# Kernel tuning notes

Measured on AMD Instinct MI355X. Metric: run time of the kernel, lower is better.

## Reference

```python
import jax, jax.numpy as jnp
import numpy as np

N = 100000      # nodes
E = 3200000     # edges
IN_DIM = 128
HID = 128
OUT_DIM = 1
LAYERS = 8
ALPHA = 0.1
THETA = 0.5


def setup_inputs() -> dict:
    key = jax.random.key(0)
    ks = jax.random.split(key, 8)
    x = jax.random.normal(ks[0], (N, IN_DIM), dtype=jnp.float32)
    edge_index = jax.random.randint(ks[1], (2, E), 0, N, dtype=jnp.int64)
    edge_weight = jax.random.uniform(ks[2], (E,), dtype=jnp.float32)  # unused by original forward path
    W_in = jax.random.normal(ks[3], (IN_DIM, HID), dtype=jnp.float32) * 0.05
    b_in = jnp.zeros((HID,), dtype=jnp.float32)
    W_gcn = jax.random.normal(ks[4], (LAYERS, HID, HID), dtype=jnp.float32) * 0.05
    W_out = jax.random.normal(ks[5], (HID, OUT_DIM), dtype=jnp.float32) * 0.05
    b_out = jnp.zeros((OUT_DIM,), dtype=jnp.float32)
    return {"x": x, "edge_weight": edge_weight, "W_in": W_in, "b_in": b_in,
            "W_gcn": W_gcn, "W_out": W_out, "b_out": b_out, "edge_index": edge_index}


def _gcn_norm(edge_index, dtype):
    # add self loops (fill value 1), symmetric normalization deg^-1/2 A deg^-1/2
    sl = jnp.arange(N, dtype=edge_index.dtype)
    row = jnp.concatenate([edge_index[0], sl])
    col = jnp.concatenate([edge_index[1], sl])
    w = jnp.ones(row.shape[0], dtype=dtype)
    deg = jax.ops.segment_sum(w, col, num_segments=N)
    dinv = jnp.where(deg > 0, jax.lax.rsqrt(deg), 0.0)
    norm = dinv[row] * dinv[col]
    return row, col, norm


def reference(x, edge_weight, W_in, b_in, W_gcn, W_out, b_out, edge_index):
    row, col, norm = _gcn_norm(edge_index, x.dtype)
    h = x @ W_in + b_in            # initial_proj
    h0 = h                          # residual x0
    for i in range(LAYERS):
        # dropout is identity in eval mode
        msg = h[row] * norm[:, None]                       # gather + scale [E+N, HID]
        agg = jax.ops.segment_sum(msg, col, num_segments=N)
        s = (1.0 - ALPHA) * agg + ALPHA * h0               # identity-mapped residual
        beta = float(np.log(THETA / (i + 1) + 1.0))
        h = (1.0 - beta) * s + beta * (s @ W_gcn[i])       # GCNII weight mix
        h = jax.nn.relu(h)
    return h @ W_out + b_out
```

## Files before the change

kernel.cpp:

```cpp
#include <hip/hip_runtime.h>
#include <hip/hip_bf16.h>
#include <math.h>

#define N_NODES 100000
#define N_EDGES 3200000
#define HID 128
#define LAYERS 8
#define ALPHA 0.1f
#define THETA 0.5f

#define SCAN_TILE 1024
#define NB_SCAN ((N_NODES + SCAN_TILE - 1) / SCAN_TILE)

typedef unsigned int uint;
typedef unsigned short ushort;
typedef __attribute__((ext_vector_type(8))) short short8;
typedef __attribute__((ext_vector_type(4))) float f32x4;

__device__ inline float bf_lo(uint p) { return __uint_as_float(p << 16); }
__device__ inline float bf_hi(uint p) { return __uint_as_float(p & 0xffff0000u); }
__device__ inline uint bf_pack(float x, float y) {
    uint ux = __float_as_uint(x), uy = __float_as_uint(y);
    uint rx = (ux + 0x7fffu + ((ux >> 16) & 1u)) >> 16;
    uint ry = (uy + 0x7fffu + ((uy >> 16) & 1u)) >> 16;
    return rx | (ry << 16);
}
__device__ inline ushort bfr(float x) {
    uint u = __float_as_uint(x);
    return (ushort)((u + 0x7fffu + ((u >> 16) & 1u)) >> 16);
}
__device__ inline float bff(ushort s) { return __uint_as_float(((uint)s) << 16); }

__global__ __launch_bounds__(256) void k_count(const int* __restrict__ col,
                                               int* __restrict__ cnt) {
    int e = blockIdx.x * 256 + threadIdx.x;
    if (e < N_EDGES) atomicAdd(&cnt[col[e]], 1);
}

__global__ __launch_bounds__(256) void k_dinv(const int* __restrict__ cnt,
                                              float* __restrict__ dinv) {
    int n = blockIdx.x * 256 + threadIdx.x;
    if (n < N_NODES) dinv[n] = rsqrtf((float)(cnt[n] + 1));
}

__global__ __launch_bounds__(256) void k_scan1(const int* __restrict__ cnt,
                                               int* __restrict__ indptr,
                                               int* __restrict__ bsum) {
    __shared__ int lds[256];
    int t = threadIdx.x;
    int base = blockIdx.x * SCAN_TILE + t * 4;
    int v[4];
    int s = 0;
#pragma unroll
    for (int j = 0; j < 4; ++j) {
        v[j] = (base + j < N_NODES) ? cnt[base + j] : 0;
        s += v[j];
    }
    lds[t] = s;
    __syncthreads();
    for (int off = 1; off < 256; off <<= 1) {
        int u = (t >= off) ? lds[t - off] : 0;
        __syncthreads();
        lds[t] += u;
        __syncthreads();
    }
    int run = lds[t] - s;
#pragma unroll
    for (int j = 0; j < 4; ++j) {
        if (base + j < N_NODES) indptr[base + j] = run;
        run += v[j];
    }
    if (t == 255) bsum[blockIdx.x] = lds[255];
}

__global__ __launch_bounds__(256) void k_scan2(const int* __restrict__ bsum,
                                               int* __restrict__ boff) {
    __shared__ int lds[256];
    int t = threadIdx.x;
    int v = (t < NB_SCAN) ? bsum[t] : 0;
    lds[t] = v;
    __syncthreads();
    for (int off = 1; off < 256; off <<= 1) {
        int u = (t >= off) ? lds[t - off] : 0;
        __syncthreads();
        lds[t] += u;
        __syncthreads();
    }
    boff[t] = lds[t] - v;
}

__global__ __launch_bounds__(256) void k_scan3(int* __restrict__ indptr,
                                               const int* __restrict__ boff) {
    int base = blockIdx.x * SCAN_TILE + threadIdx.x * 4;
    int add = boff[blockIdx.x];
#pragma unroll
    for (int j = 0; j < 4; ++j) {
        if (base + j < N_NODES) indptr[base + j] += add;
    }
    if (blockIdx.x == 0 && threadIdx.x == 0) indptr[N_NODES] = N_EDGES;
}

__global__ __launch_bounds__(256) void k_fill(const int* __restrict__ rowi,
                                              const int* __restrict__ coli,
                                              const float* __restrict__ dinv,
                                              const int* __restrict__ indptr,
                                              int* __restrict__ cursor,
                                              int2* __restrict__ csr) {
    int e = blockIdx.x * 256 + threadIdx.x;
    if (e >= N_EDGES) return;
    int r = rowi[e];
    int c = coli[e];
    int p = indptr[c] + atomicAdd(&cursor[c], 1);
    csr[p] = make_int2(r, __float_as_int(dinv[r] * dinv[c]));
}

__global__ __launch_bounds__(256) void k_wprep(const float* __restrict__ Wg,
                                               ushort* __restrict__ Wt) {
    int l = blockIdx.x;
    const float* W = Wg + (size_t)l * HID * HID;
    ushort* T = Wt + (size_t)l * HID * HID;
    int t = threadIdx.x;
#pragma unroll
    for (int i = 0; i < 16; ++i) {
        int idx = t + 256 * i;
        int k = idx >> 5;
        int c4 = idx & 31;
        float4 v = *(const float4*)(W + (size_t)k * HID + c4 * 4);
        T[(c4 * 4 + 0) * HID + k] = bfr(v.x);
        T[(c4 * 4 + 1) * HID + k] = bfr(v.y);
        T[(c4 * 4 + 2) * HID + k] = bfr(v.z);
        T[(c4 * 4 + 3) * HID + k] = bfr(v.w);
    }
}

__global__ __launch_bounds__(256) void k_spmm(const uint* __restrict__ h,
                                              const uint* __restrict__ h0,
                                              const float* __restrict__ dinv,
                                              const int* __restrict__ indptr,
                                              const int2* __restrict__ csr,
                                              uint* __restrict__ s_out) {
    int node = blockIdx.x * 4 + (threadIdx.x >> 6);
    if (node >= N_NODES) return;
    int lane = threadIdx.x & 63;
    int beg = indptr[node];
    int end = indptr[node + 1];
    float di = dinv[node];
    uint hs = h[node * 64 + lane];
    uint h0v = h0[node * 64 + lane];
    float ax[8], ay[8];
#pragma unroll
    for (int j = 0; j < 8; ++j) { ax[j] = 0.f; ay[j] = 0.f; }
    int e = beg;
    for (; e + 16 <= end; e += 16) {
        int2 rr[16];
#pragma unroll
        for (int j = 0; j < 16; ++j) rr[j] = csr[e + j];
        uint p[16];
#pragma unroll
        for (int j = 0; j < 16; ++j) p[j] = h[rr[j].x * 64 + lane];
#pragma unroll
        for (int j = 0; j < 16; ++j) {
            float w = __int_as_float(rr[j].y);
            ax[j & 7] = fmaf(w, bf_lo(p[j]), ax[j & 7]);
            ay[j & 7] = fmaf(w, bf_hi(p[j]), ay[j & 7]);
        }
    }
    for (; e < end; e += 4) {
        int2 rr[4];
        float w[4];
#pragma unroll
        for (int j = 0; j < 4; ++j) {
            int idx = e + j;
            rr[j] = csr[idx < end ? idx : beg];
            w[j] = (idx < end) ? __int_as_float(rr[j].y) : 0.f;
        }
        uint p[4];
#pragma unroll
        for (int j = 0; j < 4; ++j) p[j] = h[rr[j].x * 64 + lane];
#pragma unroll
        for (int j = 0; j < 4; ++j) {
            ax[j] = fmaf(w[j], bf_lo(p[j]), ax[j]);
            ay[j] = fmaf(w[j], bf_hi(p[j]), ay[j]);
        }
    }
    float sum0 = ((ax[0] + ax[1]) + (ax[2] + ax[3])) + ((ax[4] + ax[5]) + (ax[6] + ax[7]));
    float sum1 = ((ay[0] + ay[1]) + (ay[2] + ay[3])) + ((ay[4] + ay[5]) + (ay[6] + ay[7]));
    float selfw = di * di;
    float rx = (1.0f - ALPHA) * fmaf(selfw, bf_lo(hs), sum0) + ALPHA * bf_lo(h0v);
    float ry = (1.0f - ALPHA) * fmaf(selfw, bf_hi(hs), sum1) + ALPHA * bf_hi(h0v);
    s_out[node * 64 + lane] = bf_pack(rx, ry);
}

__global__ __launch_bounds__(256) void k_gemm_in(const float* __restrict__ A,
                                                 const float* __restrict__ W,
                                                 const float* __restrict__ bias,
                                                 uint* __restrict__ out0,
                                                 uint* __restrict__ out1) {
    __shared__ float sT[32 * 64];
    __shared__ float Ws[32 * 128];
    int t = threadIdx.x;
    int tr = t & 15;
    int tc = t >> 4;
    int rowBase = blockIdx.x * 64;
    float acc[4][8] = {};

    for (int ko = 0; ko < HID; ko += 32) {
#pragma unroll
        for (int pass = 0; pass < 2; ++pass) {
            int lin = t + 256 * pass;
            int r = lin >> 3;
            int kq = lin & 7;
            int ar = rowBase + r;
            if (ar >= N_NODES) ar = N_NODES - 1;
            float4 v = *(const float4*)(A + (size_t)ar * HID + ko + 4 * kq);
            sT[(4 * kq + 0) * 64 + r] = v.x;
            sT[(4 * kq + 1) * 64 + r] = v.y;
            sT[(4 * kq + 2) * 64 + r] = v.z;
            sT[(4 * kq + 3) * 64 + r] = v.w;
        }
#pragma unroll
        for (int pass = 0; pass < 4; ++pass) {
            int lin = t + 256 * pass;
            int k = lin >> 5;
            int c4 = lin & 31;
            *(float4*)&Ws[k * 128 + 4 * c4] =
                *(const float4*)(W + (size_t)(ko + k) * HID + 4 * c4);
        }
        __syncthreads();
#pragma unroll
        for (int k = 0; k < 32; ++k) {
            float4 a = *(const float4*)&sT[k * 64 + 4 * tr];
            float4 w0 = *(const float4*)&Ws[k * 128 + 8 * tc];
            float4 w1 = *(const float4*)&Ws[k * 128 + 8 * tc + 4];
            float av[4] = {a.x, a.y, a.z, a.w};
            float wv[8] = {w0.x, w0.y, w0.z, w0.w, w1.x, w1.y, w1.z, w1.w};
#pragma unroll
            for (int i = 0; i < 4; ++i)
#pragma unroll
                for (int j = 0; j < 8; ++j)
                    acc[i][j] = fmaf(av[i], wv[j], acc[i][j]);
        }
        __syncthreads();
    }

    int c0 = 8 * tc;
    float bb[8];
#pragma unroll
    for (int j = 0; j < 8; ++j) bb[j] = bias[c0 + j];
#pragma unroll
    for (int i = 0; i < 4; ++i) {
        int r = rowBase + 4 * tr + i;
        if (r >= N_NODES) break;
        float v[8];
#pragma unroll
        for (int j = 0; j < 8; ++j) v[j] = acc[i][j] + bb[j];
        uint4 o;
        o.x = bf_pack(v[0], v[1]);
        o.y = bf_pack(v[2], v[3]);
        o.z = bf_pack(v[4], v[5]);
        o.w = bf_pack(v[6], v[7]);
        *(uint4*)(out0 + (size_t)r * 64 + c0 / 2) = o;
        *(uint4*)(out1 + (size_t)r * 64 + c0 / 2) = o;
    }
}

#define SAS 136

__global__ __launch_bounds__(256) void k_gemm_layer(const uint* __restrict__ A,
                                                    const ushort* __restrict__ Wt,
                                                    uint* __restrict__ out0,
                                                    float beta) {
    __shared__ ushort sA[64 * SAS];
    __shared__ ushort sW[128 * SAS];
    int t = threadIdx.x;
    int lane = t & 63;
    int wv = t >> 6;
    int rowBase = blockIdx.x * 64;

#pragma unroll
    for (int i = 0; i < 4; ++i) {
        int idx = t + 256 * i;
        int r = idx >> 4;
        int q = idx & 15;
        int ar = rowBase + r;
        if (ar >= N_NODES) ar = N_NODES - 1;
        uint4 v = *(const uint4*)(A + (size_t)ar * 64 + q * 4);
        *(uint4*)((uint*)(sA + r * SAS) + q * 4) = v;
    }
#pragma unroll
    for (int i = 0; i < 8; ++i) {
        int idx = t + 256 * i;
        int r = idx >> 4;
        int q = idx & 15;
        uint4 v = *(const uint4*)((const uint*)(Wt + (size_t)r * HID) + q * 4);
        *(uint4*)((uint*)(sW + r * SAS) + q * 4) = v;
    }
    __syncthreads();

    int fr = lane & 15;
    int fq = lane >> 4;
    f32x4 acc[4][2] = {};
#pragma unroll
    for (int kc = 0; kc < 4; ++kc) {
        int kof = kc * 32 + fq * 8;
        short8 b0 = *(const short8*)(sW + (wv * 32 + fr) * SAS + kof);
        short8 b1 = *(const short8*)(sW + (wv * 32 + 16 + fr) * SAS + kof);
#pragma unroll
        for (int tm = 0; tm < 4; ++tm) {
            short8 a = *(const short8*)(sA + (tm * 16 + fr) * SAS + kof);
            acc[tm][0] = __builtin_amdgcn_mfma_f32_16x16x32_bf16(a, b0, acc[tm][0], 0, 0, 0);
            acc[tm][1] = __builtin_amdgcn_mfma_f32_16x16x32_bf16(a, b1, acc[tm][1], 0, 0, 0);
        }
    }
    __syncthreads();

    ushort* pack = sW;
    float ob = 1.0f - beta;
#pragma unroll
    for (int tm = 0; tm < 4; ++tm)
#pragma unroll
        for (int tn = 0; tn < 2; ++tn)
#pragma unroll
            for (int r = 0; r < 4; ++r) {
                int row = tm * 16 + fq * 4 + r;
                int col = wv * 32 + tn * 16 + fr;
                float sv = bff(sA[row * SAS + col]);
                float val = fmaxf(fmaf(ob, sv, beta * acc[tm][tn][r]), 0.f);
                pack[row * 128 + col] = bfr(val);
            }
    __syncthreads();
#pragma unroll
    for (int i = 0; i < 4; ++i) {
        int idx = t + 256 * i;
        int r = idx >> 4;
        int q = idx & 15;
        int ar = rowBase + r;
        if (ar < N_NODES)
            *(uint4*)(out0 + (size_t)ar * 64 + q * 4) =
                *(const uint4*)((const uint*)(pack + r * 128) + q * 4);
    }
}

__global__ __launch_bounds__(256) void k_out(const uint* __restrict__ h,
                                             const float* __restrict__ W_out,
                                             const float* __restrict__ b_out,
                                             float* __restrict__ out) {
    int node = blockIdx.x * 4 + (threadIdx.x >> 6);
    if (node >= N_NODES) return;
    int lane = threadIdx.x & 63;
    uint p = h[node * 64 + lane];
    float2 wv = *(const float2*)(W_out + lane * 2);
    float pr = bf_lo(p) * wv.x + bf_hi(p) * wv.y;
#pragma unroll
    for (int off = 32; off > 0; off >>= 1) pr += __shfl_down(pr, off);
    if (lane == 0) out[node] = pr + b_out[0];
}

extern "C" void kernel_launch(void* const* d_in, const int* in_sizes, int n_in,
                              void* d_out, int out_size, void* d_ws, size_t ws_size,
                              hipStream_t stream) {
    const float* x     = (const float*)d_in[0];
    const float* W_in  = (const float*)d_in[2];
    const float* b_in  = (const float*)d_in[3];
    const float* W_gcn = (const float*)d_in[4];
    const float* W_out = (const float*)d_in[5];
    const float* b_out = (const float*)d_in[6];
    const int*   ei    = (const int*)d_in[7];
    const int* rowi = ei;
    const int* coli = ei + N_EDGES;
    float* out = (float*)d_out;

    char* ws = (char*)d_ws;
    auto alloc = [&](size_t bytes) -> char* {
        char* p = ws;
        ws += (bytes + 255) & ~(size_t)255;
        return p;
    };
    int*    cnt     = (int*)   alloc((size_t)N_NODES * 4);
    float*  dinv    = (float*) alloc((size_t)N_NODES * 4);
    int*    indptr  = (int*)   alloc((size_t)(N_NODES + 1) * 4);
    int*    cursor  = (int*)   alloc((size_t)N_NODES * 4);
    int*    bsum    = (int*)   alloc(1024 * 4);
    int*    boff    = (int*)   alloc(1024 * 4);
    int2*   csr     = (int2*)  alloc((size_t)N_EDGES * 8);
    ushort* Wt      = (ushort*)alloc((size_t)LAYERS * HID * HID * 2);
    uint*   hA      = (uint*)  alloc((size_t)N_NODES * 64 * 4);
    uint*   hB      = (uint*)  alloc((size_t)N_NODES * 64 * 4);
    uint*   h0      = (uint*)  alloc((size_t)N_NODES * 64 * 4);

    hipMemsetAsync(cnt, 0, (size_t)N_NODES * 4, stream);
    hipMemsetAsync(cursor, 0, (size_t)N_NODES * 4, stream);

    k_count<<<(N_EDGES + 255) / 256, 256, 0, stream>>>(coli, cnt);
    k_dinv<<<(N_NODES + 255) / 256, 256, 0, stream>>>(cnt, dinv);
    k_scan1<<<NB_SCAN, 256, 0, stream>>>(cnt, indptr, bsum);
    k_scan2<<<1, 256, 0, stream>>>(bsum, boff);
    k_scan3<<<NB_SCAN, 256, 0, stream>>>(indptr, boff);
    k_fill<<<(N_EDGES + 255) / 256, 256, 0, stream>>>(rowi, coli, dinv, indptr,
                                                      cursor, csr);
    k_wprep<<<LAYERS, 256, 0, stream>>>(W_gcn, Wt);

    int gemm_blocks = (N_NODES + 63) / 64;
    k_gemm_in<<<gemm_blocks, 256, 0, stream>>>(x, W_in, b_in, h0, hA);

    for (int l = 0; l < LAYERS; ++l) {
        k_spmm<<<(N_NODES + 3) / 4, 256, 0, stream>>>(hA, h0, dinv, indptr,
                                                      csr, hB);
        float beta = logf(THETA / (float)(l + 1) + 1.0f);
        k_gemm_layer<<<gemm_blocks, 256, 0, stream>>>(
            hB, Wt + (size_t)l * HID * HID, hA, beta);
    }
    k_out<<<(N_NODES + 3) / 4, 256, 0, stream>>>(hA, W_out, b_out, out);
}
```

Measured before the change: 1.517 ms.

## Fuse SpMM aggregation with per-layer GEMM and pack CSR entries into 32 bits

Each layer now runs one kernel. Every block aggregates 64 nodes' neighbour sums straight into LDS and then does the MFMA weight mix on that tile, so the intermediate s tensor no longer makes a round trip through global memory. CSR entries shrink from int2 to a single uint: a 17-bit source index plus the bf16 normalisation weight with its sign bit dropped, which halves edge-list traffic per layer. In exchange, the 52KB of LDS per block and each wave serially gathering for 16 nodes may lower occupancy and the latency hiding the gather phase depends on. The edge weights are also stored at reduced bf16 precision.

Measured after the change: 1.849 ms. +21.9%, slower.

```diff
diff --git a/kernel.cpp b/kernel.cpp
--- a/kernel.cpp
+++ b/kernel.cpp
@@ -30,6 +30,8 @@
     return (ushort)((u + 0x7fffu + ((u >> 16) & 1u)) >> 16);
 }
 __device__ inline float bff(ushort s) { return __uint_as_float(((uint)s) << 16); }
+
+__device__ inline float rec_w(uint k) { return __uint_as_float((k >> 17) << 16); }
 
 __global__ __launch_bounds__(256) void k_count(const int* __restrict__ col,
                                                int* __restrict__ cnt) {
@@ -105,13 +107,14 @@
                                               const float* __restrict__ dinv,
                                               const int* __restrict__ indptr,
                                               int* __restrict__ cursor,
-                                              int2* __restrict__ csr) {
+                                              uint* __restrict__ csr4) {
     int e = blockIdx.x * 256 + threadIdx.x;
     if (e >= N_EDGES) return;
     int r = rowi[e];
     int c = coli[e];
     int p = indptr[c] + atomicAdd(&cursor[c], 1);
-    csr[p] = make_int2(r, __float_as_int(dinv[r] * dinv[c]));
+    float nrm = dinv[r] * dinv[c];
+    csr4[p] = (uint)r | ((uint)bfr(nrm) << 17);
 }
 
 __global__ __launch_bounds__(256) void k_wprep(const float* __restrict__ Wg,
@@ -133,62 +136,128 @@
     }
 }
 
-__global__ __launch_bounds__(256) void k_spmm(const uint* __restrict__ h,
-                                              const uint* __restrict__ h0,
-                                              const float* __restrict__ dinv,
-                                              const int* __restrict__ indptr,
-                                              const int2* __restrict__ csr,
-                                              uint* __restrict__ s_out) {
-    int node = blockIdx.x * 4 + (threadIdx.x >> 6);
-    if (node >= N_NODES) return;
-    int lane = threadIdx.x & 63;
-    int beg = indptr[node];
-    int end = indptr[node + 1];
-    float di = dinv[node];
-    uint hs = h[node * 64 + lane];
-    uint h0v = h0[node * 64 + lane];
-    float ax[8], ay[8];
-#pragma unroll
-    for (int j = 0; j < 8; ++j) { ax[j] = 0.f; ay[j] = 0.f; }
-    int e = beg;
-    for (; e + 16 <= end; e += 16) {
-        int2 rr[16];
-#pragma unroll
-        for (int j = 0; j < 16; ++j) rr[j] = csr[e + j];
-        uint p[16];
-#pragma unroll
-        for (int j = 0; j < 16; ++j) p[j] = h[rr[j].x * 64 + lane];
-#pragma unroll
-        for (int j = 0; j < 16; ++j) {
-            float w = __int_as_float(rr[j].y);
-            ax[j & 7] = fmaf(w, bf_lo(p[j]), ax[j & 7]);
-            ay[j & 7] = fmaf(w, bf_hi(p[j]), ay[j & 7]);
-        }
-    }
-    for (; e < end; e += 4) {
-        int2 rr[4];
-        float w[4];
-#pragma unroll
-        for (int j = 0; j < 4; ++j) {
-            int idx = e + j;
-            rr[j] = csr[idx < end ? idx : beg];
-            w[j] = (idx < end) ? __int_as_float(rr[j].y) : 0.f;
-        }
-        uint p[4];
-#pragma unroll
-        for (int j = 0; j < 4; ++j) p[j] = h[rr[j].x * 64 + lane];
-#pragma unroll
-        for (int j = 0; j < 4; ++j) {
-            ax[j] = fmaf(w[j], bf_lo(p[j]), ax[j]);
-            ay[j] = fmaf(w[j], bf_hi(p[j]), ay[j]);
-        }
-    }
-    float sum0 = ((ax[0] + ax[1]) + (ax[2] + ax[3])) + ((ax[4] + ax[5]) + (ax[6] + ax[7]));
-    float sum1 = ((ay[0] + ay[1]) + (ay[2] + ay[3])) + ((ay[4] + ay[5]) + (ay[6] + ay[7]));
-    float selfw = di * di;
-    float rx = (1.0f - ALPHA) * fmaf(selfw, bf_lo(hs), sum0) + ALPHA * bf_lo(h0v);
-    float ry = (1.0f - ALPHA) * fmaf(selfw, bf_hi(hs), sum1) + ALPHA * bf_hi(h0v);
-    s_out[node * 64 + lane] = bf_pack(rx, ry);
+#define SAS 136
+
+__global__ __launch_bounds__(256) void k_layer(const uint* __restrict__ h,
+                                               const uint* __restrict__ h0,
+                                               const float* __restrict__ dinv,
+                                               const int* __restrict__ indptr,
+                                               const uint* __restrict__ csr4,
+                                               const ushort* __restrict__ Wt,
+                                               uint* __restrict__ hOut,
+                                               float beta) {
+    __shared__ ushort sA[64 * SAS];
+    __shared__ ushort sW[128 * SAS];
+    int t = threadIdx.x;
+    int lane = t & 63;
+    int wv = t >> 6;
+    int nb = blockIdx.x * 64;
+
+#pragma unroll
+    for (int i = 0; i < 8; ++i) {
+        int idx = t + 256 * i;
+        int r = idx >> 4;
+        int q = idx & 15;
+        uint4 v = *(const uint4*)((const uint*)(Wt + (size_t)r * HID) + q * 4);
+        *(uint4*)((uint*)(sW + r * SAS) + q * 4) = v;
+    }
+
+    for (int i = 0; i < 16; ++i) {
+        int row = wv * 16 + i;
+        int node = nb + row;
+        int nc = node < N_NODES ? node : N_NODES - 1;
+        int beg = indptr[nc];
+        int end = indptr[nc + 1];
+        float di = dinv[nc];
+        uint hs = h[nc * 64 + lane];
+        uint h0v = h0[nc * 64 + lane];
+        float ax[8], ay[8];
+#pragma unroll
+        for (int j = 0; j < 8; ++j) { ax[j] = 0.f; ay[j] = 0.f; }
+        int e = beg;
+        for (; e + 16 <= end; e += 16) {
+            uint kk[16];
+#pragma unroll
+            for (int j = 0; j < 16; ++j) kk[j] = csr4[e + j];
+            uint p[16];
+#pragma unroll
+            for (int j = 0; j < 16; ++j) p[j] = h[(kk[j] & 0x1FFFF) * 64 + lane];
+#pragma unroll
+            for (int j = 0; j < 16; ++j) {
+                float w = rec_w(kk[j]);
+                ax[j & 7] = fmaf(w, bf_lo(p[j]), ax[j & 7]);
+                ay[j & 7] = fmaf(w, bf_hi(p[j]), ay[j & 7]);
+            }
+        }
+        for (; e < end; e += 4) {
+            uint kk[4];
+            float w[4];
+#pragma unroll
+            for (int j = 0; j < 4; ++j) {
+                int idx = e + j;
+                kk[j] = csr4[idx < end ? idx : beg];
+                w[j] = (idx < end) ? rec_w(kk[j]) : 0.f;
+            }
+            uint p[4];
+#pragma unroll
+            for (int j = 0; j < 4; ++j) p[j] = h[(kk[j] & 0x1FFFF) * 64 + lane];
+#pragma unroll
+            for (int j = 0; j < 4; ++j) {
+                ax[j] = fmaf(w[j], bf_lo(p[j]), ax[j]);
+                ay[j] = fmaf(w[j], bf_hi(p[j]), ay[j]);
+            }
+        }
+        float sum0 = ((ax[0] + ax[1]) + (ax[2] + ax[3])) + ((ax[4] + ax[5]) + (ax[6] + ax[7]));
+        float sum1 = ((ay[0] + ay[1]) + (ay[2] + ay[3])) + ((ay[4] + ay[5]) + (ay[6] + ay[7]));
+        float selfw = di * di;
+        float rx = (1.0f - ALPHA) * fmaf(selfw, bf_lo(hs), sum0) + ALPHA * bf_lo(h0v);
+        float ry = (1.0f - ALPHA) * fmaf(selfw, bf_hi(hs), sum1) + ALPHA * bf_hi(h0v);
+        *((uint*)(sA + row * SAS) + lane) = bf_pack(rx, ry);
+    }
+    __syncthreads();
+
+    int fr = lane & 15;
+    int fq = lane >> 4;
+    f32x4 acc[4][2] = {};
+#pragma unroll
+    for (int kc = 0; kc < 4; ++kc) {
+        int kof = kc * 32 + fq * 8;
+        short8 b0 = *(const short8*)(sW + (wv * 32 + fr) * SAS + kof);
+        short8 b1 = *(const short8*)(sW + (wv * 32 + 16 + fr) * SAS + kof);
+#pragma unroll
+        for (int tm = 0; tm < 4; ++tm) {
+            short8 a = *(const short8*)(sA + (tm * 16 + fr) * SAS + kof);
+            acc[tm][0] = __builtin_amdgcn_mfma_f32_16x16x32_bf16(a, b0, acc[tm][0], 0, 0, 0);
+            acc[tm][1] = __builtin_amdgcn_mfma_f32_16x16x32_bf16(a, b1, acc[tm][1], 0, 0, 0);
+        }
+    }
+    __syncthreads();
+
+    ushort* pack = sW;
+    float ob = 1.0f - beta;
+#pragma unroll
+    for (int tm = 0; tm < 4; ++tm)
+#pragma unroll
+        for (int tn = 0; tn < 2; ++tn)
+#pragma unroll
+            for (int r = 0; r < 4; ++r) {
+                int row = tm * 16 + fq * 4 + r;
+                int col = wv * 32 + tn * 16 + fr;
+                float sv = bff(sA[row * SAS + col]);
+                float val = fmaxf(fmaf(ob, sv, beta * acc[tm][tn][r]), 0.f);
+                pack[row * 128 + col] = bfr(val);
+            }
+    __syncthreads();
+#pragma unroll
+    for (int i = 0; i < 4; ++i) {
+        int idx = t + 256 * i;
+        int r = idx >> 4;
+        int q = idx & 15;
+        int ar = nb + r;
+        if (ar < N_NODES)
+            *(uint4*)(hOut + (size_t)ar * 64 + q * 4) =
+                *(const uint4*)((const uint*)(pack + r * 128) + q * 4);
+    }
 }
 
 __global__ __launch_bounds__(256) void k_gemm_in(const float* __restrict__ A,
@@ -261,83 +330,6 @@
         o.w = bf_pack(v[6], v[7]);
         *(uint4*)(out0 + (size_t)r * 64 + c0 / 2) = o;
         *(uint4*)(out1 + (size_t)r * 64 + c0 / 2) = o;
-    }
-}
-
-#define SAS 136
-
-__global__ __launch_bounds__(256) void k_gemm_layer(const uint* __restrict__ A,
-                                                    const ushort* __restrict__ Wt,
-                                                    uint* __restrict__ out0,
-                                                    float beta) {
-    __shared__ ushort sA[64 * SAS];
-    __shared__ ushort sW[128 * SAS];
-    int t = threadIdx.x;
-    int lane = t & 63;
-    int wv = t >> 6;
-    int rowBase = blockIdx.x * 64;
-
-#pragma unroll
-    for (int i = 0; i < 4; ++i) {
-        int idx = t + 256 * i;
-        int r = idx >> 4;
-        int q = idx & 15;
-        int ar = rowBase + r;
-        if (ar >= N_NODES) ar = N_NODES - 1;
-        uint4 v = *(const uint4*)(A + (size_t)ar * 64 + q * 4);
-        *(uint4*)((uint*)(sA + r * SAS) + q * 4) = v;
-    }
-#pragma unroll
-    for (int i = 0; i < 8; ++i) {
-        int idx = t + 256 * i;
-        int r = idx >> 4;
-        int q = idx & 15;
-        uint4 v = *(const uint4*)((const uint*)(Wt + (size_t)r * HID) + q * 4);
-        *(uint4*)((uint*)(sW + r * SAS) + q * 4) = v;
-    }
-    __syncthreads();
-
-    int fr = lane & 15;
-    int fq = lane >> 4;
-    f32x4 acc[4][2] = {};
-#pragma unroll
-    for (int kc = 0; kc < 4; ++kc) {
-        int kof = kc * 32 + fq * 8;
-        short8 b0 = *(const short8*)(sW + (wv * 32 + fr) * SAS + kof);
-        short8 b1 = *(const short8*)(sW + (wv * 32 + 16 + fr) * SAS + kof);
-#pragma unroll
-        for (int tm = 0; tm < 4; ++tm) {
-            short8 a = *(const short8*)(sA + (tm * 16 + fr) * SAS + kof);
-            acc[tm][0] = __builtin_amdgcn_mfma_f32_16x16x32_bf16(a, b0, acc[tm][0], 0, 0, 0);
-            acc[tm][1] = __builtin_amdgcn_mfma_f32_16x16x32_bf16(a, b1, acc[tm][1], 0, 0, 0);
-        }
-    }
-    __syncthreads();
-
-    ushort* pack = sW;
-    float ob = 1.0f - beta;
-#pragma unroll
-    for (int tm = 0; tm < 4; ++tm)
-#pragma unroll
-        for (int tn = 0; tn < 2; ++tn)
-#pragma unroll
-            for (int r = 0; r < 4; ++r) {
-                int row = tm * 16 + fq * 4 + r;
-                int col = wv * 32 + tn * 16 + fr;
-                float sv = bff(sA[row * SAS + col]);
-                float val = fmaxf(fmaf(ob, sv, beta * acc[tm][tn][r]), 0.f);
-                pack[row * 128 + col] = bfr(val);
-            }
-    __syncthreads();
-#pragma unroll
-    for (int i = 0; i < 4; ++i) {
-        int idx = t + 256 * i;
-        int r = idx >> 4;
-        int q = idx & 15;
-        int ar = rowBase + r;
-        if (ar < N_NODES)
-            *(uint4*)(out0 + (size_t)ar * 64 + q * 4) =
-                *(const uint4*)((const uint*)(pack + r * 128) + q * 4);
     }
 }
 
@@ -382,7 +374,7 @@
     int*    cursor  = (int*)   alloc((size_t)N_NODES * 4);
     int*    bsum    = (int*)   alloc(1024 * 4);
     int*    boff    = (int*)   alloc(1024 * 4);
-    int2*   csr     = (int2*)  alloc((size_t)N_EDGES * 8);
+    uint*   csr4    = (uint*)  alloc((size_t)N_EDGES * 4);
     ushort* Wt      = (ushort*)alloc((size_t)LAYERS * HID * HID * 2);
     uint*   hA      = (uint*)  alloc((size_t)N_NODES * 64 * 4);
     uint*   hB      = (uint*)  alloc((size_t)N_NODES * 64 * 4);
@@ -397,18 +389,19 @@
     k_scan2<<<1, 256, 0, stream>>>(bsum, boff);
     k_scan3<<<NB_SCAN, 256, 0, stream>>>(indptr, boff);
     k_fill<<<(N_EDGES + 255) / 256, 256, 0, stream>>>(rowi, coli, dinv, indptr,
-                                                      cursor, csr);
+                                                      cursor, csr4);
     k_wprep<<<LAYERS, 256, 0, stream>>>(W_gcn, Wt);
 
-    int gemm_blocks = (N_NODES + 63) / 64;
-    k_gemm_in<<<gemm_blocks, 256, 0, stream>>>(x, W_in, b_in, h0, hA);
+    int tile_blocks = (N_NODES + 63) / 64;
+    k_gemm_in<<<tile_blocks, 256, 0, stream>>>(x, W_in, b_in, h0, hA);
 
     for (int l = 0; l < LAYERS; ++l) {
-        k_spmm<<<(N_NODES + 3) / 4, 256, 0, stream>>>(hA, h0, dinv, indptr,
-                                                      csr, hB);
+        const uint* hin = (l & 1) ? hB : hA;
+        uint* hout      = (l & 1) ? hA : hB;
         float beta = logf(THETA / (float)(l + 1) + 1.0f);
-        k_gemm_layer<<<gemm_blocks, 256, 0, stream>>>(
-            hB, Wt + (size_t)l * HID * HID, hA, beta);
+        k_layer<<<tile_blocks, 256, 0, stream>>>(hin, h0, dinv, indptr, csr4,
+                                                 Wt + (size_t)l * HID * HID,
+                                                 hout, beta);
     }
     k_out<<<(N_NODES + 3) / 4, 256, 0, stream>>>(hA, W_out, b_out, out);
 }
```
